# Performance work log

Measured on AMD Instinct MI355X. Metric: run time of the kernel, lower is better.

Reference implementation:

```python
import jax, jax.numpy as jnp
import numpy as np

N_NODES = 50000
N_GROUPS = 512
D_FEAT = 128
D_HID = 128
N_CLASS = 16
NEG_SLOPE = 0.2


def gat_conv(x, edge_index, W, a_src, a_dst, bias, n):
    """Single-head PyG-style GATConv (with self-loops, eval mode / no dropout)."""
    h = x @ W  # [n, D_HID]
    loop = jnp.arange(n)
    src = jnp.concatenate([edge_index[0], loop])  # neighbors j
    dst = jnp.concatenate([edge_index[1], loop])  # targets i
    a_s = h @ a_src  # [n]
    a_d = h @ a_dst  # [n]
    e = jax.nn.leaky_relu(a_s[src] + a_d[dst], NEG_SLOPE)  # [E+n]
    # segment softmax over incoming edges of each dst node
    m = jax.ops.segment_max(e, dst, num_segments=n)
    e = jnp.exp(e - m[dst])
    denom = jax.ops.segment_sum(e, dst, num_segments=n)
    alpha = e / denom[dst]
    out = jax.ops.segment_sum(alpha[:, None] * h[src], dst, num_segments=n)
    return out + bias


def setup_inputs() -> dict:
    key = jax.random.key(0)
    ks = jax.random.split(key, 12)
    s_f = 1.0 / np.sqrt(D_FEAT)
    s_h = 1.0 / np.sqrt(D_HID)
    return {
        "x_full": jax.random.normal(ks[0], (N_NODES, D_FEAT), jnp.float32),
        "x_group": jax.random.normal(ks[1], (N_GROUPS, D_FEAT), jnp.float32),
        "W_full": jax.random.normal(ks[2], (D_FEAT, D_HID), jnp.float32) * s_f,
        "a_src_full": jax.random.normal(ks[3], (D_HID,), jnp.float32) * s_h,
        "a_dst_full": jax.random.normal(ks[4], (D_HID,), jnp.float32) * s_h,
        "bias_full": jnp.zeros((D_HID,), jnp.float32),
        "W_group": jax.random.normal(ks[5], (D_FEAT, D_HID), jnp.float32) * s_f,
        "a_src_group": jax.random.normal(ks[6], (D_HID,), jnp.float32) * s_h,
        "a_dst_group": jax.random.normal(ks[7], (D_HID,), jnp.float32) * s_h,
        "bias_group": jnp.zeros((D_HID,), jnp.float32),
        "fc_W": jax.random.normal(ks[8], (D_HID, N_CLASS), jnp.float32) * s_h,
        "fc_b": jnp.zeros((N_CLASS,), jnp.float32),
        "edge_index_full": jax.random.randint(ks[9], (2, 600000), 0, N_NODES, jnp.int64),
        "edge_index_group": jax.random.randint(ks[10], (2, 4096), 0, N_GROUPS, jnp.int64),
        "node_group": jax.random.randint(ks[11], (N_NODES,), 0, N_GROUPS, jnp.int64),
    }


def reference(x_full, x_group, W_full, a_src_full, a_dst_full, bias_full,
              W_group, a_src_group, a_dst_group, bias_group, fc_W, fc_b,
              edge_index_full, edge_index_group, node_group):
    full_x = jax.nn.elu(gat_conv(x_full, edge_index_full, W_full, a_src_full,
                                 a_dst_full, bias_full, N_NODES))   # [N, D_HID]
    group_x = jax.nn.elu(gat_conv(x_group, edge_index_group, W_group, a_src_group,
                                  a_dst_group, bias_group, N_GROUPS))  # [G, D_HID]

    # mean feature of groups adjacent to each group (edges src->dst in group graph)
    gsrc, gdst = edge_index_group[0], edge_index_group[1]
    adj_sum = jax.ops.segment_sum(group_x[gdst], gsrc, num_segments=N_GROUPS)
    cnt = jax.ops.segment_sum(jnp.ones_like(gsrc, jnp.float32), gsrc, num_segments=N_GROUPS)
    adj_mean = adj_sum / jnp.maximum(cnt, 1.0)[:, None]  # [G, D_HID]

    gf = group_x[node_group]   # group feature per node, [N, D_HID]
    am = adj_mean[node_group]  # adjacent-group mean per node, [N, D_HID]

    # dot(node, group_feature) and mean_j dot(node, adj_j) == dot(node, adj_mean)
    iw_group = jnp.sum(full_x * gf, axis=-1, keepdims=True)  # [N, 1]
    iw_adj = jnp.sum(full_x * am, axis=-1, keepdims=True)    # [N, 1]

    updated = full_x + iw_group * gf + iw_adj * am  # [N, D_HID]
    out = updated @ fc_W + fc_b                     # [N, N_CLASS]
    return (out, updated)
```

## Files before the change

kernel.cpp:

```cpp
#include <hip/hip_runtime.h>

typedef unsigned short u16;
typedef unsigned int u32;

static __device__ __forceinline__ float lrelu(float x) { return x >= 0.f ? x : 0.2f * x; }

static __device__ __forceinline__ u16 f2bf(float f) {
    u32 u = __float_as_uint(f);
    u += 0x7FFF + ((u >> 16) & 1);
    return (u16)(u >> 16);
}
static __device__ __forceinline__ float bf2f(u16 h) {
    return __uint_as_float((u32)h << 16);
}

__global__ __launch_bounds__(256) void gemm128_kernel(const float* __restrict__ X,
                                                      const float* __restrict__ W,
                                                      const float* __restrict__ a_src,
                                                      const float* __restrict__ a_dst,
                                                      u16* __restrict__ Hb,
                                                      float* __restrict__ as_out,
                                                      float* __restrict__ ad_out, int N) {
    __shared__ float Ws[64 * 128];
    __shared__ float Xs[32 * 128];
    int tid = threadIdx.x;
    long base = (long)blockIdx.x * 32;
    float4* Ws4 = (float4*)Ws;
    float4* Xs4 = (float4*)Xs;
    const float4* X4 = (const float4*)(X + base * 128);
    for (int i = tid; i < 1024; i += 256) {
        int r = i >> 5;
        Xs4[i] = (base + r < N) ? X4[i] : make_float4(0.f, 0.f, 0.f, 0.f);
    }
    int fgrp = tid & 31;
    int n0 = (tid >> 5) * 4;
    float4 acc[4] = {};
    for (int half = 0; half < 2; ++half) {
        __syncthreads();
        const float4* W4 = (const float4*)(W + half * 64 * 128);
        for (int i = tid; i < 2048; i += 256) Ws4[i] = W4[i];
        __syncthreads();
        #pragma unroll 4
        for (int kk = 0; kk < 64; ++kk) {
            float4 w = Ws4[kk * 32 + fgrp];
            #pragma unroll
            for (int j = 0; j < 4; ++j) {
                float x = Xs[(n0 + j) * 128 + half * 64 + kk];
                acc[j].x += x * w.x; acc[j].y += x * w.y;
                acc[j].z += x * w.z; acc[j].w += x * w.w;
            }
        }
    }
    float4 as4 = ((const float4*)a_src)[fgrp];
    float4 ad4 = ((const float4*)a_dst)[fgrp];
    float ps[4], pd[4];
    #pragma unroll
    for (int j = 0; j < 4; ++j) {
        ps[j] = acc[j].x * as4.x + acc[j].y * as4.y + acc[j].z * as4.z + acc[j].w * as4.w;
        pd[j] = acc[j].x * ad4.x + acc[j].y * ad4.y + acc[j].z * ad4.z + acc[j].w * ad4.w;
    }
    #pragma unroll
    for (int off = 16; off; off >>= 1) {
        #pragma unroll
        for (int j = 0; j < 4; ++j) {
            ps[j] += __shfl_xor(ps[j], off);
            pd[j] += __shfl_xor(pd[j], off);
        }
    }
    if ((tid & 31) == 0) {
        #pragma unroll
        for (int j = 0; j < 4; ++j) {
            long n = base + n0 + j;
            if (n < N) { as_out[n] = ps[j]; ad_out[n] = pd[j]; }
        }
    }
    #pragma unroll
    for (int j = 0; j < 4; ++j) {
        long n = base + n0 + j;
        if (n < N) {
            ushort4 hv;
            hv.x = f2bf(acc[j].x); hv.y = f2bf(acc[j].y);
            hv.z = f2bf(acc[j].z); hv.w = f2bf(acc[j].w);
            ((ushort4*)(Hb + n * 128))[fgrp] = hv;
        }
    }
}

__global__ __launch_bounds__(256) void hist2_kernel(const int* __restrict__ efd, int E, int N,
                                                    const int* __restrict__ egd, int Eg, int G,
                                                    int Npad, int* __restrict__ deg) {
    int i = blockIdx.x * 256 + threadIdx.x;
    int totF = E + N;
    int tot = totF + Eg + G;
    if (i >= tot) return;
    int d;
    if (i < E) d = efd[i];
    else if (i < totF) d = i - E;
    else {
        int j = i - totF;
        d = Npad + ((j < Eg) ? egd[j] : (j - Eg));
    }
    atomicAdd(&deg[d], 1);
}

__global__ __launch_bounds__(256) void scan1_kernel(const int* __restrict__ deg, int n,
                                                    int* __restrict__ bsum) {
    __shared__ int s[256];
    int i = blockIdx.x * 256 + threadIdx.x;
    s[threadIdx.x] = (i < n) ? deg[i] : 0;
    __syncthreads();
    for (int off = 128; off; off >>= 1) {
        if (threadIdx.x < off) s[threadIdx.x] += s[threadIdx.x + off];
        __syncthreads();
    }
    if (threadIdx.x == 0) bsum[blockIdx.x] = s[0];
}

__global__ __launch_bounds__(256) void scan2_kernel(int* __restrict__ bsum, int nb,
                                                    int* __restrict__ offs, int Ltot) {
    __shared__ int s[256];
    int t = threadIdx.x;
    int v = (t < nb) ? bsum[t] : 0;
    s[t] = v;
    __syncthreads();
    for (int off = 1; off < 256; off <<= 1) {
        int u = (t >= off) ? s[t - off] : 0;
        __syncthreads();
        s[t] += u;
        __syncthreads();
    }
    if (t < nb) bsum[t] = s[t] - v;
    if (t == nb - 1) offs[Ltot] = s[t];
}

__global__ __launch_bounds__(256) void scan3_kernel(int* __restrict__ deg, int n,
                                                    const int* __restrict__ bsum,
                                                    int* __restrict__ offs) {
    __shared__ int s[256];
    int i = blockIdx.x * 256 + threadIdx.x;
    int v = (i < n) ? deg[i] : 0;
    s[threadIdx.x] = v;
    __syncthreads();
    for (int off = 1; off < 256; off <<= 1) {
        int t = (threadIdx.x >= off) ? s[threadIdx.x - off] : 0;
        __syncthreads();
        s[threadIdx.x] += t;
        __syncthreads();
    }
    if (i < n) {
        int excl = s[threadIdx.x] - v + bsum[blockIdx.x];
        offs[i] = excl;
        deg[i] = excl;
    }
}

__global__ __launch_bounds__(256) void place2_kernel(const int* __restrict__ efs,
                                                     const int* __restrict__ efd, int E, int N,
                                                     const int* __restrict__ egs,
                                                     const int* __restrict__ egd, int Eg, int G,
                                                     int Npad,
                                                     const float* __restrict__ a_s,
                                                     const float* __restrict__ a_d,
                                                     const float* __restrict__ a_sg,
                                                     const float* __restrict__ a_dg,
                                                     int* __restrict__ cursor,
                                                     int* __restrict__ slot,
                                                     float* __restrict__ eslot) {
    int i = blockIdx.x * 256 + threadIdx.x;
    int totF = E + N;
    int tot = totF + Eg + G;
    if (i >= tot) return;
    int s, d, dcur;
    float av;
    if (i < totF) {
        if (i < E) { s = efs[i]; d = efd[i]; } else { s = d = i - E; }
        av = a_s[s] + a_d[d];
        dcur = d;
    } else {
        int j = i - totF;
        if (j < Eg) { s = egs[j]; d = egd[j]; } else { s = d = j - Eg; }
        av = a_sg[s] + a_dg[d];
        dcur = Npad + d;
    }
    float e = expf(lrelu(av));
    int pos = atomicAdd(&cursor[dcur], 1);
    slot[pos] = s;
    eslot[pos] = e;
}

__global__ __launch_bounds__(256) void pull2_kernel(const u16* __restrict__ Hf,
                                                    const u16* __restrict__ Hg,
                                                    const int* __restrict__ offs,
                                                    const int* __restrict__ slot,
                                                    const float* __restrict__ eslot,
                                                    const float* __restrict__ bias_f,
                                                    const float* __restrict__ bias_g,
                                                    float* __restrict__ fx,
                                                    float* __restrict__ gx,
                                                    int N, int G, int Npad) {
    int gid = blockIdx.x * 256 + threadIdx.x;
    int w = gid >> 6, lane = gid & 63;
    const u16* H;
    const float* bias;
    float* out;
    int idx;
    if (w < N) {
        H = Hf; bias = bias_f; out = fx + (long)w * 128; idx = w;
    } else if (w < N + G) {
        int g = w - N;
        H = Hg; bias = bias_g; out = gx + (long)g * 128; idx = Npad + g;
    } else return;
    int beg = offs[idx], end = offs[idx + 1];
    float accx = 0.f, accy = 0.f, ssum = 0.f;
    int k = beg;
    for (; k + 2 <= end; k += 2) {
        int s0 = slot[k], s1 = slot[k + 1];
        float e0 = eslot[k], e1 = eslot[k + 1];
        ushort2 h0 = ((const ushort2*)H)[(long)s0 * 64 + lane];
        ushort2 h1 = ((const ushort2*)H)[(long)s1 * 64 + lane];
        accx += e0 * bf2f(h0.x) + e1 * bf2f(h1.x);
        accy += e0 * bf2f(h0.y) + e1 * bf2f(h1.y);
        ssum += e0 + e1;
    }
    if (k < end) {
        int s0 = slot[k];
        float e0 = eslot[k];
        ushort2 h0 = ((const ushort2*)H)[(long)s0 * 64 + lane];
        accx += e0 * bf2f(h0.x);
        accy += e0 * bf2f(h0.y);
        ssum += e0;
    }
    float inv = 1.f / ssum;
    float2 b = ((const float2*)bias)[lane];
    float ox = accx * inv + b.x;
    float oy = accy * inv + b.y;
    ox = ox > 0.f ? ox : expm1f(ox);
    oy = oy > 0.f ? oy : expm1f(oy);
    ((float2*)out)[lane] = make_float2(ox, oy);
}

__global__ __launch_bounds__(256) void adj_kernel(const int* __restrict__ gsrc,
                                                  const int* __restrict__ gdst, int Eg,
                                                  const float* __restrict__ gx,
                                                  float* __restrict__ adj_sum,
                                                  float* __restrict__ cnt) {
    int gid = blockIdx.x * 256 + threadIdx.x;
    int i = gid >> 6, lane = gid & 63;
    if (i >= Eg) return;
    int s = gsrc[i], d = gdst[i];
    float2 gv = ((const float2*)gx)[(long)d * 64 + lane];
    atomicAdd(&adj_sum[(long)s * 128 + 2 * lane], gv.x);
    atomicAdd(&adj_sum[(long)s * 128 + 2 * lane + 1], gv.y);
    if (lane == 0) atomicAdd(&cnt[s], 1.f);
}

__global__ __launch_bounds__(256) void final_kernel(const int* __restrict__ node_group,
                                                    const float* __restrict__ gx,
                                                    const float* __restrict__ adj_sum,
                                                    const float* __restrict__ cnt,
                                                    const float* __restrict__ fcW,
                                                    const float* __restrict__ fcb,
                                                    float* __restrict__ upd,
                                                    float* __restrict__ out, int N) {
    int gid = blockIdx.x * 256 + threadIdx.x;
    int n = gid >> 6, lane = gid & 63;
    if (n >= N) return;
    int g = node_group[n];
    float2 row = ((const float2*)upd)[(long)n * 64 + lane];
    float2 gf = ((const float2*)gx)[(long)g * 64 + lane];
    float inv_cnt = 1.f / fmaxf(cnt[g], 1.f);
    float2 amv = ((const float2*)adj_sum)[(long)g * 64 + lane];
    float amx = amv.x * inv_cnt, amy = amv.y * inv_cnt;
    float pg = row.x * gf.x + row.y * gf.y;
    float pa = row.x * amx + row.y * amy;
    for (int off = 32; off; off >>= 1) {
        pg += __shfl_xor(pg, off);
        pa += __shfl_xor(pa, off);
    }
    float ux = row.x + pg * gf.x + pa * amx;
    float uy = row.y + pg * gf.y + pa * amy;
    ((float2*)upd)[(long)n * 64 + lane] = make_float2(ux, uy);
    float p[16];
    const float4* fW4 = (const float4*)fcW;
    #pragma unroll
    for (int q = 0; q < 4; ++q) {
        float4 w0 = fW4[(2 * lane) * 4 + q];
        float4 w1 = fW4[(2 * lane + 1) * 4 + q];
        p[4 * q + 0] = ux * w0.x + uy * w1.x;
        p[4 * q + 1] = ux * w0.y + uy * w1.y;
        p[4 * q + 2] = ux * w0.z + uy * w1.z;
        p[4 * q + 3] = ux * w0.w + uy * w1.w;
    }
    #pragma unroll
    for (int off = 32; off; off >>= 1) {
        #pragma unroll
        for (int c = 0; c < 16; ++c) p[c] += __shfl_xor(p[c], off);
    }
    if (lane == 0) {
        const float4* fb4 = (const float4*)fcb;
        float4* o4 = (float4*)(out + (long)n * 16);
        #pragma unroll
        for (int q = 0; q < 4; ++q) {
            float4 b = fb4[q];
            float4 o;
            o.x = p[4 * q + 0] + b.x;
            o.y = p[4 * q + 1] + b.y;
            o.z = p[4 * q + 2] + b.z;
            o.w = p[4 * q + 3] + b.w;
            o4[q] = o;
        }
    }
}

extern "C" void kernel_launch(void* const* d_in, const int* in_sizes, int n_in,
                              void* d_out, int out_size, void* d_ws, size_t ws_size,
                              hipStream_t stream) {
    const float* x_full = (const float*)d_in[0];
    const float* x_group = (const float*)d_in[1];
    const float* W_full = (const float*)d_in[2];
    const float* a_src_full = (const float*)d_in[3];
    const float* a_dst_full = (const float*)d_in[4];
    const float* bias_full = (const float*)d_in[5];
    const float* W_group = (const float*)d_in[6];
    const float* a_src_g = (const float*)d_in[7];
    const float* a_dst_g = (const float*)d_in[8];
    const float* bias_g = (const float*)d_in[9];
    const float* fc_W = (const float*)d_in[10];
    const float* fc_b = (const float*)d_in[11];
    const int* ef = (const int*)d_in[12];
    const int* eg = (const int*)d_in[13];
    const int* node_group = (const int*)d_in[14];

    int N = in_sizes[0] / 128;
    int G = in_sizes[1] / 128;
    int E = in_sizes[12] / 2;
    int Eg = in_sizes[13] / 2;
    const int* ef_src = ef;
    const int* ef_dst = ef + E;
    const int* eg_src = eg;
    const int* eg_dst = eg + Eg;

    int Npad = (N + 255) & ~255;
    int Ltot = Npad + G;
    int LtotPad = (Ltot + 255) & ~255;
    int totF = E + N;
    int tot = totF + Eg + G;

    float* out_cls = (float*)d_out;
    float* fx = out_cls + (long)N * 16;

    char* w = (char*)d_ws;
    auto alloc = [&](size_t bytes) {
        char* p = w;
        w += (bytes + 255) & ~(size_t)255;
        return p;
    };
    u16* h_full = (u16*)alloc((size_t)N * 128 * 2);
    u16* h_g = (u16*)alloc((size_t)G * 128 * 2);
    float* a_s = (float*)alloc((size_t)N * 4);
    float* a_d = (float*)alloc((size_t)N * 4);
    float* a_sg = (float*)alloc((size_t)G * 4);
    float* a_dg = (float*)alloc((size_t)G * 4);
    float* gx = (float*)alloc((size_t)G * 128 * 4);
    float* adj_sum = (float*)alloc((size_t)G * 128 * 4);
    float* cnt = (float*)alloc((size_t)G * 4);
    int* deg = (int*)alloc((size_t)LtotPad * 4);
    int* offs = (int*)alloc((size_t)(LtotPad + 1) * 4);
    int* slot = (int*)alloc((size_t)tot * 4);
    float* eslot = (float*)alloc((size_t)tot * 4);
    int* bsum = (int*)alloc(256 * 4);

    (void)hipMemsetAsync(deg, 0, (size_t)LtotPad * 4, stream);
    (void)hipMemsetAsync(adj_sum, 0, (size_t)G * 128 * 4 + (size_t)G * 4, stream);

    auto cdiv = [](int a, int b) { return (a + b - 1) / b; };

    gemm128_kernel<<<cdiv(N, 32), 256, 0, stream>>>(x_full, W_full, a_src_full, a_dst_full,
                                                    h_full, a_s, a_d, N);
    gemm128_kernel<<<cdiv(G, 32), 256, 0, stream>>>(x_group, W_group, a_src_g, a_dst_g,
                                                    h_g, a_sg, a_dg, G);

    int nb = cdiv(Ltot, 256);
    hist2_kernel<<<cdiv(tot, 256), 256, 0, stream>>>(ef_dst, E, N, eg_dst, Eg, G, Npad, deg);
    scan1_kernel<<<nb, 256, 0, stream>>>(deg, Ltot, bsum);
    scan2_kernel<<<1, 256, 0, stream>>>(bsum, nb, offs, Ltot);
    scan3_kernel<<<nb, 256, 0, stream>>>(deg, Ltot, bsum, offs);
    place2_kernel<<<cdiv(tot, 256), 256, 0, stream>>>(ef_src, ef_dst, E, N, eg_src, eg_dst,
                                                      Eg, G, Npad, a_s, a_d, a_sg, a_dg,
                                                      deg, slot, eslot);

    pull2_kernel<<<cdiv((N + G) * 64, 256), 256, 0, stream>>>(h_full, h_g, offs, slot, eslot,
                                                              bias_full, bias_g, fx, gx,
                                                              N, G, Npad);

    adj_kernel<<<cdiv(Eg * 64, 256), 256, 0, stream>>>(eg_src, eg_dst, Eg, gx, adj_sum, cnt);
    final_kernel<<<cdiv(N * 64, 256), 256, 0, stream>>>(node_group, gx, adj_sum, cnt, fc_W,
                                                        fc_b, fx, out_cls, N);
}
```

Before: 329.5 us.

## Merge GEMM launches, fold scan2 into scan3, combine memsets, transpose-reduce FC

Both GEMMs now run in one launch that picks full or group operands per block. The single-block scan2 step is dropped: each scan3 block rescans the block sums itself. The two memsets become one contiguous memset from adj_sum through deg, which relies on those buffers being adjacent in the workspace. The final FC reduction now uses a transpose-style butterfly so each group of lanes writes one class, cutting shuffle count; together these aim to remove launch overhead and redundant shuffles.

```diff
diff --git a/kernel.cpp b/kernel.cpp
--- a/kernel.cpp
+++ b/kernel.cpp
@@ -14,23 +14,32 @@
     return __uint_as_float((u32)h << 16);
 }
 
-__global__ __launch_bounds__(256) void gemm128_kernel(const float* __restrict__ X,
-                                                      const float* __restrict__ W,
-                                                      const float* __restrict__ a_src,
-                                                      const float* __restrict__ a_dst,
-                                                      u16* __restrict__ Hb,
-                                                      float* __restrict__ as_out,
-                                                      float* __restrict__ ad_out, int N) {
+__global__ __launch_bounds__(256) void gemm_both_kernel(
+        const float* __restrict__ Xf, const float* __restrict__ Wf,
+        const float* __restrict__ asf, const float* __restrict__ adf,
+        u16* __restrict__ Hbf, float* __restrict__ as_f, float* __restrict__ ad_f, int N,
+        const float* __restrict__ Xg, const float* __restrict__ Wg,
+        const float* __restrict__ asg, const float* __restrict__ adg,
+        u16* __restrict__ Hbg, float* __restrict__ as_g, float* __restrict__ ad_g, int G,
+        int nbFull) {
+    const float* X; const float* W; const float* av; const float* dv;
+    u16* Hb; float* as_out; float* ad_out; int n_lim; long base;
+    if (blockIdx.x < nbFull) {
+        X = Xf; W = Wf; av = asf; dv = adf; Hb = Hbf; as_out = as_f; ad_out = ad_f;
+        n_lim = N; base = (long)blockIdx.x * 32;
+    } else {
+        X = Xg; W = Wg; av = asg; dv = adg; Hb = Hbg; as_out = as_g; ad_out = ad_g;
+        n_lim = G; base = (long)(blockIdx.x - nbFull) * 32;
+    }
     __shared__ float Ws[64 * 128];
     __shared__ float Xs[32 * 128];
     int tid = threadIdx.x;
-    long base = (long)blockIdx.x * 32;
     float4* Ws4 = (float4*)Ws;
     float4* Xs4 = (float4*)Xs;
     const float4* X4 = (const float4*)(X + base * 128);
     for (int i = tid; i < 1024; i += 256) {
         int r = i >> 5;
-        Xs4[i] = (base + r < N) ? X4[i] : make_float4(0.f, 0.f, 0.f, 0.f);
+        Xs4[i] = (base + r < n_lim) ? X4[i] : make_float4(0.f, 0.f, 0.f, 0.f);
     }
     int fgrp = tid & 31;
     int n0 = (tid >> 5) * 4;
@@ -51,8 +60,8 @@
             }
         }
     }
-    float4 as4 = ((const float4*)a_src)[fgrp];
-    float4 ad4 = ((const float4*)a_dst)[fgrp];
+    float4 as4 = ((const float4*)av)[fgrp];
+    float4 ad4 = ((const float4*)dv)[fgrp];
     float ps[4], pd[4];
     #pragma unroll
     for (int j = 0; j < 4; ++j) {
@@ -71,13 +80,13 @@
         #pragma unroll
         for (int j = 0; j < 4; ++j) {
             long n = base + n0 + j;
-            if (n < N) { as_out[n] = ps[j]; ad_out[n] = pd[j]; }
+            if (n < n_lim) { as_out[n] = ps[j]; ad_out[n] = pd[j]; }
         }
     }
     #pragma unroll
     for (int j = 0; j < 4; ++j) {
         long n = base + n0 + j;
-        if (n < N) {
+        if (n < n_lim) {
             ushort4 hv;
             hv.x = f2bf(acc[j].x); hv.y = f2bf(acc[j].y);
             hv.z = f2bf(acc[j].z); hv.w = f2bf(acc[j].w);
@@ -116,11 +125,25 @@
     if (threadIdx.x == 0) bsum[blockIdx.x] = s[0];
 }
 
-__global__ __launch_bounds__(256) void scan2_kernel(int* __restrict__ bsum, int nb,
+__global__ __launch_bounds__(256) void scan3_kernel(int* __restrict__ deg, int n, int nb,
+                                                    const int* __restrict__ bsum,
                                                     int* __restrict__ offs, int Ltot) {
+    __shared__ int sb[256];
     __shared__ int s[256];
     int t = threadIdx.x;
-    int v = (t < nb) ? bsum[t] : 0;
+    sb[t] = (t < nb) ? bsum[t] : 0;
+    __syncthreads();
+    for (int off = 1; off < 256; off <<= 1) {
+        int u = (t >= off) ? sb[t - off] : 0;
+        __syncthreads();
+        sb[t] += u;
+        __syncthreads();
+    }
+    int blockOff = (blockIdx.x == 0) ? 0 : sb[blockIdx.x - 1];
+    if (blockIdx.x == 0 && t == 0) offs[Ltot] = sb[nb - 1];
+
+    int i = blockIdx.x * 256 + t;
+    int v = (i < n) ? deg[i] : 0;
     s[t] = v;
     __syncthreads();
     for (int off = 1; off < 256; off <<= 1) {
@@ -129,26 +152,8 @@
         s[t] += u;
         __syncthreads();
     }
-    if (t < nb) bsum[t] = s[t] - v;
-    if (t == nb - 1) offs[Ltot] = s[t];
-}
-
-__global__ __launch_bounds__(256) void scan3_kernel(int* __restrict__ deg, int n,
-                                                    const int* __restrict__ bsum,
-                                                    int* __restrict__ offs) {
-    __shared__ int s[256];
-    int i = blockIdx.x * 256 + threadIdx.x;
-    int v = (i < n) ? deg[i] : 0;
-    s[threadIdx.x] = v;
-    __syncthreads();
-    for (int off = 1; off < 256; off <<= 1) {
-        int t = (threadIdx.x >= off) ? s[threadIdx.x - off] : 0;
-        __syncthreads();
-        s[threadIdx.x] += t;
-        __syncthreads();
-    }
     if (i < n) {
-        int excl = s[threadIdx.x] - v + bsum[blockIdx.x];
+        int excl = s[t] - v + blockOff;
         offs[i] = excl;
         deg[i] = excl;
     }
@@ -273,6 +278,7 @@
     float amx = amv.x * inv_cnt, amy = amv.y * inv_cnt;
     float pg = row.x * gf.x + row.y * gf.y;
     float pa = row.x * amx + row.y * amy;
+    #pragma unroll
     for (int off = 32; off; off >>= 1) {
         pg += __shfl_xor(pg, off);
         pa += __shfl_xor(pa, off);
@@ -280,36 +286,35 @@
     float ux = row.x + pg * gf.x + pa * amx;
     float uy = row.y + pg * gf.y + pa * amy;
     ((float2*)upd)[(long)n * 64 + lane] = make_float2(ux, uy);
-    float p[16];
+
+    float v[16];
     const float4* fW4 = (const float4*)fcW;
     #pragma unroll
     for (int q = 0; q < 4; ++q) {
         float4 w0 = fW4[(2 * lane) * 4 + q];
         float4 w1 = fW4[(2 * lane + 1) * 4 + q];
-        p[4 * q + 0] = ux * w0.x + uy * w1.x;
-        p[4 * q + 1] = ux * w0.y + uy * w1.y;
-        p[4 * q + 2] = ux * w0.z + uy * w1.z;
-        p[4 * q + 3] = ux * w0.w + uy * w1.w;
-    }
-    #pragma unroll
-    for (int off = 32; off; off >>= 1) {
+        v[4 * q + 0] = ux * w0.x + uy * w1.x;
+        v[4 * q + 1] = ux * w0.y + uy * w1.y;
+        v[4 * q + 2] = ux * w0.z + uy * w1.z;
+        v[4 * q + 3] = ux * w0.w + uy * w1.w;
+    }
+    #pragma unroll
+    for (int stage = 0; stage < 4; ++stage) {
+        int width = 32 >> stage;
+        int half = 8 >> stage;
+        bool hi = (lane & width) != 0;
         #pragma unroll
-        for (int c = 0; c < 16; ++c) p[c] += __shfl_xor(p[c], off);
-    }
-    if (lane == 0) {
-        const float4* fb4 = (const float4*)fcb;
-        float4* o4 = (float4*)(out + (long)n * 16);
-        #pragma unroll
-        for (int q = 0; q < 4; ++q) {
-            float4 b = fb4[q];
-            float4 o;
-            o.x = p[4 * q + 0] + b.x;
-            o.y = p[4 * q + 1] + b.y;
-            o.z = p[4 * q + 2] + b.z;
-            o.w = p[4 * q + 3] + b.w;
-            o4[q] = o;
+        for (int c = 0; c < half; ++c) {
+            float send = hi ? v[c] : v[c + half];
+            float recv = __shfl_xor(send, width);
+            float keep = hi ? v[c + half] : v[c];
+            v[c] = keep + recv;
         }
     }
+    v[0] += __shfl_xor(v[0], 1);
+    v[0] += __shfl_xor(v[0], 2);
+    int cls = (lane >> 2) & 15;
+    if ((lane & 3) == 0) out[(long)n * 16 + cls] = v[0] + fcb[cls];
 }
 
 extern "C" void kernel_launch(void* const* d_in, const int* in_sizes, int n_in,
@@ -370,21 +375,20 @@
     float* eslot = (float*)alloc((size_t)tot * 4);
     int* bsum = (int*)alloc(256 * 4);
 
-    (void)hipMemsetAsync(deg, 0, (size_t)LtotPad * 4, stream);
-    (void)hipMemsetAsync(adj_sum, 0, (size_t)G * 128 * 4 + (size_t)G * 4, stream);
+    size_t zero_span = (char*)(deg + LtotPad) - (char*)adj_sum;
+    (void)hipMemsetAsync(adj_sum, 0, zero_span, stream);
 
     auto cdiv = [](int a, int b) { return (a + b - 1) / b; };
 
-    gemm128_kernel<<<cdiv(N, 32), 256, 0, stream>>>(x_full, W_full, a_src_full, a_dst_full,
-                                                    h_full, a_s, a_d, N);
-    gemm128_kernel<<<cdiv(G, 32), 256, 0, stream>>>(x_group, W_group, a_src_g, a_dst_g,
-                                                    h_g, a_sg, a_dg, G);
+    int nbFull = cdiv(N, 32);
+    gemm_both_kernel<<<nbFull + cdiv(G, 32), 256, 0, stream>>>(
+        x_full, W_full, a_src_full, a_dst_full, h_full, a_s, a_d, N,
+        x_group, W_group, a_src_g, a_dst_g, h_g, a_sg, a_dg, G, nbFull);
 
     int nb = cdiv(Ltot, 256);
     hist2_kernel<<<cdiv(tot, 256), 256, 0, stream>>>(ef_dst, E, N, eg_dst, Eg, G, Npad, deg);
     scan1_kernel<<<nb, 256, 0, stream>>>(deg, Ltot, bsum);
-    scan2_kernel<<<1, 256, 0, stream>>>(bsum, nb, offs, Ltot);
-    scan3_kernel<<<nb, 256, 0, stream>>>(deg, Ltot, bsum, offs);
+    scan3_kernel<<<nb, 256, 0, stream>>>(deg, Ltot, nb, bsum, offs, Ltot);
     place2_kernel<<<cdiv(tot, 256), 256, 0, stream>>>(ef_src, ef_dst, E, N, eg_src, eg_dst,
                                                       Eg, G, Npad, a_s, a_d, a_sg, a_dg,
                                                       deg, slot, eslot);
```

Result: slower. 337.7 us (+2.5%).
